# Kernel optimization log

Hardware: AMD Instinct MI355X
Metric: run time of the kernel (lower is better)

The kernel has to match this reference:

```python
import jax, jax.numpy as jnp
import numpy as np

N = 16384
E = 524288
F_IN, F_HID, F_OUT = 128, 256, 128
EPS = 1e-5


def setup_inputs() -> dict:
    key = jax.random.key(0)
    ks = jax.random.split(key, 8)
    x = jax.random.normal(ks[0], (N, F_IN), dtype=jnp.float32)
    edge_index = jax.random.randint(ks[1], (2, E), 0, N, dtype=jnp.int64)
    edge_weight = jax.random.uniform(ks[2], (E,), dtype=jnp.float32)
    # Linear params stored as [in, out] (y = x @ W + b; same math as torch Linear)
    W1_w = jax.random.normal(ks[3], (F_IN, F_HID), dtype=jnp.float32) / np.sqrt(F_IN)
    W1_b = jnp.zeros((F_HID,), dtype=jnp.float32)
    W2_w = jax.random.normal(ks[4], (F_HID, F_OUT), dtype=jnp.float32) / np.sqrt(F_HID)
    W2_b = jnp.zeros((F_OUT,), dtype=jnp.float32)
    ln_g = jnp.ones((F_HID,), dtype=jnp.float32)
    ln_b = jnp.zeros((F_HID,), dtype=jnp.float32)
    return {"x": x, "edge_index": edge_index, "edge_weight": edge_weight,
            "W1_w": W1_w, "W1_b": W1_b, "W2_w": W2_w, "W2_b": W2_b,
            "ln_g": ln_g, "ln_b": ln_b}


def _layernorm(h, g, b):
    mu = jnp.mean(h, axis=-1, keepdims=True)
    var = jnp.var(h, axis=-1, keepdims=True)
    return (h - mu) * jax.lax.rsqrt(var + EPS) * g + b


def reference(x, edge_index, edge_weight, W1_w, W1_b, W2_w, W2_b, ln_g, ln_b):
    n = x.shape[0]
    adj = jnp.zeros((n, n), dtype=x.dtype).at[edge_index[0], edge_index[1]].set(edge_weight)
    adj = adj + jnp.eye(n, dtype=x.dtype)
    degree = jnp.clip(adj.sum(axis=1, keepdims=True), 1.0, None)
    adj = adj / degree
    h = jnp.matmul(adj, x) @ W1_w + W1_b          # [N, F_HID]
    h = jax.nn.relu(_layernorm(h, ln_g, ln_b))
    # dropout is identity in eval mode
    out = jnp.matmul(adj, h) @ W2_w + W2_b        # [N, F_OUT]
    return out
```

## Files before the change

kernel.cpp:

```cpp
#include <hip/hip_runtime.h>

#define N_NODES 16384
#define F_IN    128
#define F_HID   256
#define F_OUT   128
#define LN_EPS  1e-5f
#define CAP     128
#define H0STR   136
#define H1STR   264
#define REPSTR  132

typedef __attribute__((ext_vector_type(8))) short bf16x8;
typedef __attribute__((ext_vector_type(4))) float f32x4;
typedef __attribute__((ext_vector_type(4))) int   i32x4;

__device__ __forceinline__ unsigned short bf16rne(float f) {
    unsigned u = __float_as_uint(f);
    unsigned r = (u + 0x7fffu + ((u >> 16) & 1u)) >> 16;
    return (unsigned short)r;
}
__device__ __forceinline__ float bf_lo(unsigned v) { return __uint_as_float(v << 16); }
__device__ __forceinline__ float bf_hi(unsigned v) { return __uint_as_float(v & 0xffff0000u); }

__global__ void pre_small_kernel(int* __restrict__ cur, const unsigned* __restrict__ ei,
                                 int* __restrict__ mode) {
    int b = blockIdx.x, t = threadIdx.x;
    if (b < 64) {
        cur[b * 256 + t] = 0;
    } else {
        __shared__ int nz;
        if (t == 0) nz = 0;
        __syncthreads();
        for (int it = 0; it < 4; ++it) {
            int idx = 2 * (t + it * 256) + 1;
            if (ei[idx] != 0u) nz = 1;
        }
        __syncthreads();
        if (t == 0) *mode = (nz == 0) ? 1 : 0;
    }
}

__global__ void prep_fill_kernel(const void* __restrict__ ei, const int* __restrict__ mode,
                                 int* __restrict__ cur, int2* __restrict__ ed, int E, int nF,
                                 const float* __restrict__ x, unsigned short* __restrict__ xb,
                                 const float* __restrict__ W1, unsigned short* __restrict__ W1t,
                                 const float* __restrict__ W2, unsigned short* __restrict__ W2t) {
    int b = blockIdx.x, t = threadIdx.x;
    if (b < nF) {
        int base = b * 1024 + t;
        int m = *mode;
#pragma unroll
        for (int u = 0; u < 4; ++u) {
            int e = base + u * 256;
            if (e >= E) continue;
            int r, c;
            if (m) {
                const long long* p = (const long long*)ei;
                r = (int)p[e]; c = (int)p[e + E];
            } else {
                const int* p = (const int*)ei;
                r = p[e]; c = p[e + E];
            }
            if (((unsigned)r | (unsigned)c) >= N_NODES) continue;
            int pos = atomicAdd(&cur[r], 1);
            if (pos < CAP) ed[r * CAP + pos] = make_int2(c, e);
        }
    } else if (b < nF + 2048) {
        int i = ((b - nF) * 256 + t) * 4;
        float4 v = *(const float4*)&x[i];
        ushort4 o;
        o.x = bf16rne(v.x); o.y = bf16rne(v.y); o.z = bf16rne(v.z); o.w = bf16rne(v.w);
        *(ushort4*)&xb[i] = o;
    } else if (b < nF + 2176) {
        int id = (b - nF - 2048) * 256 + t;
        int n = id >> 7, k = id & 127;
        W1t[id] = bf16rne(W1[(size_t)k * F_HID + n]);
    } else {
        int id = (b - nF - 2176) * 256 + t;
        int n = id >> 8, k = id & 255;
        W2t[id] = bf16rne(W2[(size_t)k * F_OUT + n]);
    }
}

__launch_bounds__(1024, 8)
__global__ void agg_mlp_kernel(const float* __restrict__ ew, int* __restrict__ cur,
                               int2* __restrict__ ed, float* __restrict__ invdeg,
                               const unsigned* __restrict__ xb,
                               const unsigned short* __restrict__ W1t,
                               const unsigned short* __restrict__ W2t,
                               const float* __restrict__ b1,
                               const float* __restrict__ ln_g, const float* __restrict__ ln_b,
                               unsigned short* __restrict__ h2b) {
    __shared__ int   scol[16][CAP];
    __shared__ int   seid[16][CAP];
    __shared__ float sw[16][CAP];
    __shared__ unsigned short H0[16 * H0STR];
    __shared__ unsigned short H1[16 * H1STR];
    __shared__ float red[2][16][16];

    int t = threadIdx.x, wave = t >> 6, lane = t & 63;
    int lnid = lane & 15, quad = lane >> 4;
    int half = lane >> 5, hl = lane & 31;
    int Rbase = blockIdx.x * 16;
    int r = Rbase + wave;

    int d = cur[r];
    if (d > CAP) d = CAP;
    int dpad = (d + 15) & ~15;
    int2* row = ed + (size_t)r * CAP;
    for (int i = lane; i < d; i += 64) {
        int2 e = row[i];
        scol[wave][i] = e.x;
        seid[wave][i] = e.y;
    }
    for (int i = d + lane; i < dpad; i += 64) {
        scol[wave][i] = -2;
        seid[wave][i] = 0;
    }
    asm volatile("s_waitcnt lgkmcnt(0)" ::: "memory");

    float wsum = 0.0f;
    for (int i = lane; i < d; i += 64) {
        int myc = scol[wave][i], mye = seid[wave][i];
        bool kill = false;
        for (int jb = 0; jb < dpad; jb += 16) {
            const int* cb = &scol[wave][jb];
            const int* eb = &seid[wave][jb];
            i32x4 c0 = *(const i32x4*)(cb);
            i32x4 c1 = *(const i32x4*)(cb + 4);
            i32x4 c2 = *(const i32x4*)(cb + 8);
            i32x4 c3 = *(const i32x4*)(cb + 12);
            i32x4 e0 = *(const i32x4*)(eb);
            i32x4 e1 = *(const i32x4*)(eb + 4);
            i32x4 e2 = *(const i32x4*)(eb + 8);
            i32x4 e3 = *(const i32x4*)(eb + 12);
            kill |= (c0.x == myc && e0.x > mye);
            kill |= (c0.y == myc && e0.y > mye);
            kill |= (c0.z == myc && e0.z > mye);
            kill |= (c0.w == myc && e0.w > mye);
            kill |= (c1.x == myc && e1.x > mye);
            kill |= (c1.y == myc && e1.y > mye);
            kill |= (c1.z == myc && e1.z > mye);
            kill |= (c1.w == myc && e1.w > mye);
            kill |= (c2.x == myc && e2.x > mye);
            kill |= (c2.y == myc && e2.y > mye);
            kill |= (c2.z == myc && e2.z > mye);
            kill |= (c2.w == myc && e2.w > mye);
            kill |= (c3.x == myc && e3.x > mye);
            kill |= (c3.y == myc && e3.y > mye);
            kill |= (c3.z == myc && e3.z > mye);
            kill |= (c3.w == myc && e3.w > mye);
        }
        float w = kill ? 0.0f : ew[mye];
        sw[wave][i] = w;
        row[i] = make_int2(myc, __float_as_int(w));
        wsum += w;
    }
    asm volatile("s_waitcnt lgkmcnt(0)" ::: "memory");
    for (int off = 32; off; off >>= 1) wsum += __shfl_xor(wsum, off, 64);
    float inv = 1.0f / (1.0f + wsum);
    if (lane == 0) { invdeg[r] = inv; cur[r] = d; }

    const uint2* xb2 = (const uint2*)xb;
    uint2 sv = xb2[(size_t)r * 32 + hl];
    float selfw = half ? 0.0f : 1.0f;
    float a0 = selfw * bf_lo(sv.x), a1 = selfw * bf_hi(sv.x);
    float a2 = selfw * bf_lo(sv.y), a3 = selfw * bf_hi(sv.y);
    int j = 0;
    for (; j + 16 <= d; j += 16) {
        int c[8]; float w[8]; uint2 v[8];
#pragma unroll
        for (int u = 0; u < 8; ++u) {
            c[u] = scol[wave][j + 2 * u + half];
            w[u] = sw[wave][j + 2 * u + half];
        }
#pragma unroll
        for (int u = 0; u < 8; ++u) v[u] = xb2[(size_t)c[u] * 32 + hl];
#pragma unroll
        for (int u = 0; u < 8; ++u) {
            a0 += w[u] * bf_lo(v[u].x); a1 += w[u] * bf_hi(v[u].x);
            a2 += w[u] * bf_lo(v[u].y); a3 += w[u] * bf_hi(v[u].y);
        }
    }
    for (; j + 2 <= d; j += 2) {
        int cc = scol[wave][j + half];
        float w = sw[wave][j + half];
        uint2 v = xb2[(size_t)cc * 32 + hl];
        a0 += w * bf_lo(v.x); a1 += w * bf_hi(v.x);
        a2 += w * bf_lo(v.y); a3 += w * bf_hi(v.y);
    }
    if (j < d) {
        int cc = scol[wave][j];
        float w = half ? 0.0f : sw[wave][j];
        uint2 v = xb2[(size_t)cc * 32 + hl];
        a0 += w * bf_lo(v.x); a1 += w * bf_hi(v.x);
        a2 += w * bf_lo(v.y); a3 += w * bf_hi(v.y);
    }
    a0 += __shfl_xor(a0, 32, 64); a1 += __shfl_xor(a1, 32, 64);
    a2 += __shfl_xor(a2, 32, 64); a3 += __shfl_xor(a3, 32, 64);
    if (half == 0) {
        unsigned w0 = ((unsigned)bf16rne(a1 * inv) << 16) | (unsigned)bf16rne(a0 * inv);
        unsigned w1 = ((unsigned)bf16rne(a3 * inv) << 16) | (unsigned)bf16rne(a2 * inv);
        *(uint2*)&H0[wave * H0STR + hl * 4] = make_uint2(w0, w1);
    }
    __syncthreads();

    bf16x8 a[4];
#pragma unroll
    for (int ch = 0; ch < 4; ++ch)
        a[ch] = *(const bf16x8*)&H0[lnid * H0STR + ch * 32 + quad * 8];
    f32x4 acc = {0.0f, 0.0f, 0.0f, 0.0f};
    {
        const unsigned short* wrow = &W1t[(size_t)(wave * 16 + lnid) * F_IN];
#pragma unroll
        for (int ch = 0; ch < 4; ++ch) {
            bf16x8 b = *(const bf16x8*)&wrow[ch * 32 + quad * 8];
            acc = __builtin_amdgcn_mfma_f32_16x16x32_bf16(a[ch], b, acc, 0, 0, 0);
        }
    }
    float s[4], q[4];
    {
        float bv = b1[wave * 16 + lnid];
#pragma unroll
        for (int rr = 0; rr < 4; ++rr) {
            float v = acc[rr] + bv;
            acc[rr] = v;
            s[rr] = v; q[rr] = v * v;
        }
    }
#pragma unroll
    for (int rr = 0; rr < 4; ++rr)
        for (int off = 1; off < 16; off <<= 1) {
            s[rr] += __shfl_xor(s[rr], off, 64);
            q[rr] += __shfl_xor(q[rr], off, 64);
        }
    if (lnid == 0) {
#pragma unroll
        for (int rr = 0; rr < 4; ++rr) {
            red[0][wave][quad * 4 + rr] = s[rr];
            red[1][wave][quad * 4 + rr] = q[rr];
        }
    }
    __syncthreads();
    float mean[4], rinv[4];
#pragma unroll
    for (int rr = 0; rr < 4; ++rr) {
        int rowi = quad * 4 + rr;
        float S = 0.0f, Q = 0.0f;
#pragma unroll
        for (int w2 = 0; w2 < 16; ++w2) { S += red[0][w2][rowi]; Q += red[1][w2][rowi]; }
        mean[rr] = S * (1.0f / F_HID);
        float var = Q * (1.0f / F_HID) - mean[rr] * mean[rr];
        rinv[rr] = rsqrtf(var + LN_EPS);
    }
    {
        int c = wave * 16 + lnid;
        float g = ln_g[c], bb = ln_b[c];
#pragma unroll
        for (int rr = 0; rr < 4; ++rr) {
            float v = fmaxf((acc[rr] - mean[rr]) * rinv[rr] * g + bb, 0.0f);
            H1[(quad * 4 + rr) * H1STR + c] = bf16rne(v);
        }
    }
    __syncthreads();

    unsigned short* rep = H0;
    if (wave < 8) {
        bf16x8 a2[8];
#pragma unroll
        for (int ch = 0; ch < 8; ++ch)
            a2[ch] = *(const bf16x8*)&H1[lnid * H1STR + ch * 32 + quad * 8];
        f32x4 c2 = {0.0f, 0.0f, 0.0f, 0.0f};
        const unsigned short* wrow = &W2t[(size_t)(wave * 16 + lnid) * F_HID];
#pragma unroll
        for (int ch = 0; ch < 8; ++ch) {
            bf16x8 b = *(const bf16x8*)&wrow[ch * 32 + quad * 8];
            c2 = __builtin_amdgcn_mfma_f32_16x16x32_bf16(a2[ch], b, c2, 0, 0, 0);
        }
#pragma unroll
        for (int rr = 0; rr < 4; ++rr)
            rep[(quad * 4 + rr) * REPSTR + wave * 16 + lnid] = bf16rne(c2[rr]);
    }
    __syncthreads();

    if (t < 512) {
        int m = t >> 5, cg = t & 31;
        *(ushort4*)&h2b[(size_t)(Rbase + m) * F_OUT + cg * 4] =
            *(const ushort4*)&rep[m * REPSTR + cg * 4];
    }
}

__global__ void spmm2_kernel(const unsigned* __restrict__ xb, const int* __restrict__ cur,
                             const int2* __restrict__ ed, const float* __restrict__ invdeg,
                             const float* __restrict__ bias, float* __restrict__ outp) {
    int wave = threadIdx.x >> 6, lane = threadIdx.x & 63;
    int half = lane >> 5, hl = lane & 31;
    int r = blockIdx.x * 4 + wave;
    const int2* row = ed + (size_t)r * CAP;
    const uint2* xb2 = (const uint2*)xb;
    int d = cur[r];
    if (d > CAP) d = CAP;
    uint2 sv = xb2[(size_t)r * 32 + hl];
    float selfw = half ? 0.0f : 1.0f;
    float a0 = selfw * bf_lo(sv.x), a1 = selfw * bf_hi(sv.x);
    float a2 = selfw * bf_lo(sv.y), a3 = selfw * bf_hi(sv.y);
    int j = 0;
    for (; j + 16 <= d; j += 16) {
        int2 q[8]; uint2 v[8];
#pragma unroll
        for (int u = 0; u < 8; ++u) q[u] = row[j + 2 * u + half];
#pragma unroll
        for (int u = 0; u < 8; ++u) v[u] = xb2[(size_t)q[u].x * 32 + hl];
#pragma unroll
        for (int u = 0; u < 8; ++u) {
            float w = __int_as_float(q[u].y);
            a0 += w * bf_lo(v[u].x); a1 += w * bf_hi(v[u].x);
            a2 += w * bf_lo(v[u].y); a3 += w * bf_hi(v[u].y);
        }
    }
    for (; j + 2 <= d; j += 2) {
        int2 q = row[j + half];
        uint2 v = xb2[(size_t)q.x * 32 + hl];
        float w = __int_as_float(q.y);
        a0 += w * bf_lo(v.x); a1 += w * bf_hi(v.x);
        a2 += w * bf_lo(v.y); a3 += w * bf_hi(v.y);
    }
    if (j < d) {
        int2 q = row[j];
        float w = half ? 0.0f : __int_as_float(q.y);
        uint2 v = xb2[(size_t)q.x * 32 + hl];
        a0 += w * bf_lo(v.x); a1 += w * bf_hi(v.x);
        a2 += w * bf_lo(v.y); a3 += w * bf_hi(v.y);
    }
    a0 += __shfl_xor(a0, 32, 64); a1 += __shfl_xor(a1, 32, 64);
    a2 += __shfl_xor(a2, 32, 64); a3 += __shfl_xor(a3, 32, 64);
    if (half == 0) {
        float inv = invdeg[r];
        float4 o;
        o.x = a0 * inv + bias[4 * hl];     o.y = a1 * inv + bias[4 * hl + 1];
        o.z = a2 * inv + bias[4 * hl + 2]; o.w = a3 * inv + bias[4 * hl + 3];
        ((float4*)outp)[(size_t)r * 32 + hl] = o;
    }
}

extern "C" void kernel_launch(void* const* d_in, const int* in_sizes, int n_in,
                              void* d_out, int out_size, void* d_ws, size_t ws_size,
                              hipStream_t stream) {
    const float* x   = (const float*)d_in[0];
    const void*  ei  = d_in[1];
    const float* ew  = (const float*)d_in[2];
    const float* W1  = (const float*)d_in[3];
    const float* b1  = (const float*)d_in[4];
    const float* W2  = (const float*)d_in[5];
    const float* b2  = (const float*)d_in[6];
    const float* lng = (const float*)d_in[7];
    const float* lnb = (const float*)d_in[8];
    float* out = (float*)d_out;
    int E = in_sizes[2];

    char* w = (char*)d_ws;
    size_t off = 0;
    auto take = [&](size_t bytes) -> char* {
        char* p = w + off;
        off += (bytes + 255) & ~(size_t)255;
        return p;
    };
    int*   cur    = (int*)take((size_t)N_NODES * 4);
    float* invdeg = (float*)take((size_t)N_NODES * 4);
    int2*  ed     = (int2*)take((size_t)N_NODES * CAP * 8);
    unsigned short* xb  = (unsigned short*)take((size_t)N_NODES * F_IN * 2);
    unsigned short* h2b = (unsigned short*)take((size_t)N_NODES * F_OUT * 2);
    unsigned short* W1t = (unsigned short*)take((size_t)F_IN * F_HID * 2);
    unsigned short* W2t = (unsigned short*)take((size_t)F_HID * F_OUT * 2);
    int*   mode   = (int*)take(4);

    int nF = (E + 1023) / 1024;
    pre_small_kernel<<<65, 256, 0, stream>>>(cur, (const unsigned*)ei, mode);
    prep_fill_kernel<<<nF + 2304, 256, 0, stream>>>(ei, mode, cur, ed, E, nF,
                                                    x, xb, W1, W1t, W2, W2t);
    agg_mlp_kernel<<<N_NODES / 16, 1024, 0, stream>>>(ew, cur, ed, invdeg,
                                                      (const unsigned*)xb, W1t, W2t,
                                                      b1, lng, lnb, h2b);
    spmm2_kernel<<<N_NODES / 4, 256, 0, stream>>>((const unsigned*)h2b, cur, ed, invdeg,
                                                  b2, out);
}
```

Measured before the change: 188.2 us.

## Split bf16 feature matrices into two column planes for gather locality

Stores the bf16 x and h2 feature matrices as two 64-column planes, so each plane is half the size and more likely to stay cached during random neighbor gathers. Both SpMM passes now loop over the two planes, gathering 4-byte words instead of 8-byte words. The second SpMM is rebuilt with 1024-thread blocks that stage edge columns and weights in shared memory before gathering. The cost is twice the index/weight LDS reads, an extra pass over the edge lists, and narrower per-lane loads.

```diff
diff --git a/kernel.cpp b/kernel.cpp
--- a/kernel.cpp
+++ b/kernel.cpp
@@ -9,6 +9,7 @@
 #define H0STR   136
 #define H1STR   264
 #define REPSTR  132
+#define PLANEU  (N_NODES * 32)
 
 typedef __attribute__((ext_vector_type(8))) short bf16x8;
 typedef __attribute__((ext_vector_type(4))) float f32x4;
@@ -70,7 +71,9 @@
         float4 v = *(const float4*)&x[i];
         ushort4 o;
         o.x = bf16rne(v.x); o.y = bf16rne(v.y); o.z = bf16rne(v.z); o.w = bf16rne(v.w);
-        *(ushort4*)&xb[i] = o;
+        int n = i >> 7, f = i & 127;
+        int p = f >> 6, fo = f & 63;
+        *(ushort4*)&xb[(size_t)p * (N_NODES * 64) + n * 64 + fo] = o;
     } else if (b < nF + 2176) {
         int id = (b - nF - 2048) * 256 + t;
         int n = id >> 7, k = id & 127;
@@ -161,49 +164,47 @@
     float inv = 1.0f / (1.0f + wsum);
     if (lane == 0) { invdeg[r] = inv; cur[r] = d; }
 
-    const uint2* xb2 = (const uint2*)xb;
-    uint2 sv = xb2[(size_t)r * 32 + hl];
     float selfw = half ? 0.0f : 1.0f;
-    float a0 = selfw * bf_lo(sv.x), a1 = selfw * bf_hi(sv.x);
-    float a2 = selfw * bf_lo(sv.y), a3 = selfw * bf_hi(sv.y);
-    int j = 0;
-    for (; j + 16 <= d; j += 16) {
-        int c[8]; float w[8]; uint2 v[8];
-#pragma unroll
-        for (int u = 0; u < 8; ++u) {
-            c[u] = scol[wave][j + 2 * u + half];
-            w[u] = sw[wave][j + 2 * u + half];
-        }
-#pragma unroll
-        for (int u = 0; u < 8; ++u) v[u] = xb2[(size_t)c[u] * 32 + hl];
-#pragma unroll
-        for (int u = 0; u < 8; ++u) {
-            a0 += w[u] * bf_lo(v[u].x); a1 += w[u] * bf_hi(v[u].x);
-            a2 += w[u] * bf_lo(v[u].y); a3 += w[u] * bf_hi(v[u].y);
-        }
-    }
-    for (; j + 2 <= d; j += 2) {
-        int cc = scol[wave][j + half];
-        float w = sw[wave][j + half];
-        uint2 v = xb2[(size_t)cc * 32 + hl];
-        a0 += w * bf_lo(v.x); a1 += w * bf_hi(v.x);
-        a2 += w * bf_lo(v.y); a3 += w * bf_hi(v.y);
-    }
-    if (j < d) {
-        int cc = scol[wave][j];
-        float w = half ? 0.0f : sw[wave][j];
-        uint2 v = xb2[(size_t)cc * 32 + hl];
-        a0 += w * bf_lo(v.x); a1 += w * bf_hi(v.x);
-        a2 += w * bf_lo(v.y); a3 += w * bf_hi(v.y);
-    }
-    a0 += __shfl_xor(a0, 32, 64); a1 += __shfl_xor(a1, 32, 64);
-    a2 += __shfl_xor(a2, 32, 64); a3 += __shfl_xor(a3, 32, 64);
-    if (half == 0) {
-        unsigned w0 = ((unsigned)bf16rne(a1 * inv) << 16) | (unsigned)bf16rne(a0 * inv);
-        unsigned w1 = ((unsigned)bf16rne(a3 * inv) << 16) | (unsigned)bf16rne(a2 * inv);
-        *(uint2*)&H0[wave * H0STR + hl * 4] = make_uint2(w0, w1);
-    }
-    __syncthreads();
+#pragma unroll 1
+    for (int p = 0; p < 2; ++p) {
+        const unsigned* xp = xb + (size_t)p * PLANEU;
+        unsigned sv = xp[r * 32 + hl];
+        float a0 = selfw * bf_lo(sv), a1 = selfw * bf_hi(sv);
+        int j = 0;
+        for (; j + 16 <= d; j += 16) {
+            int c[8]; float w[8]; unsigned v[8];
+#pragma unroll
+            for (int u = 0; u < 8; ++u) {
+                c[u] = scol[wave][j + 2 * u + half];
+                w[u] = sw[wave][j + 2 * u + half];
+            }
+#pragma unroll
+            for (int u = 0; u < 8; ++u) v[u] = xp[c[u] * 32 + hl];
+#pragma unroll
+            for (int u = 0; u < 8; ++u) {
+                a0 += w[u] * bf_lo(v[u]); a1 += w[u] * bf_hi(v[u]);
+            }
+        }
+        for (; j + 2 <= d; j += 2) {
+            int cc = scol[wave][j + half];
+            float w = sw[wave][j + half];
+            unsigned v = xp[cc * 32 + hl];
+            a0 += w * bf_lo(v); a1 += w * bf_hi(v);
+        }
+        if (j < d) {
+            int cc = scol[wave][j];
+            float w = half ? 0.0f : sw[wave][j];
+            unsigned v = xp[cc * 32 + hl];
+            a0 += w * bf_lo(v); a1 += w * bf_hi(v);
+        }
+        a0 += __shfl_xor(a0, 32, 64);
+        a1 += __shfl_xor(a1, 32, 64);
+        if (half == 0) {
+            unsigned w0 = ((unsigned)bf16rne(a1 * inv) << 16) | (unsigned)bf16rne(a0 * inv);
+            *(unsigned*)&H0[wave * H0STR + p * 64 + hl * 2] = w0;
+        }
+        __syncthreads();
+    }
 
     bf16x8 a[4];
 #pragma unroll
@@ -285,61 +286,75 @@
 
     if (t < 512) {
         int m = t >> 5, cg = t & 31;
-        *(ushort4*)&h2b[(size_t)(Rbase + m) * F_OUT + cg * 4] =
+        int p = cg >> 4, fo = (cg & 15) * 4;
+        *(ushort4*)&h2b[(size_t)p * (N_NODES * 64) + (size_t)(Rbase + m) * 64 + fo] =
             *(const ushort4*)&rep[m * REPSTR + cg * 4];
     }
 }
 
+__launch_bounds__(1024, 8)
 __global__ void spmm2_kernel(const unsigned* __restrict__ xb, const int* __restrict__ cur,
                              const int2* __restrict__ ed, const float* __restrict__ invdeg,
                              const float* __restrict__ bias, float* __restrict__ outp) {
-    int wave = threadIdx.x >> 6, lane = threadIdx.x & 63;
+    __shared__ int   scol[16][CAP];
+    __shared__ float sw[16][CAP];
+    int t = threadIdx.x, wave = t >> 6, lane = t & 63;
     int half = lane >> 5, hl = lane & 31;
-    int r = blockIdx.x * 4 + wave;
+    int r = blockIdx.x * 16 + wave;
     const int2* row = ed + (size_t)r * CAP;
-    const uint2* xb2 = (const uint2*)xb;
     int d = cur[r];
     if (d > CAP) d = CAP;
-    uint2 sv = xb2[(size_t)r * 32 + hl];
+    for (int i = lane; i < d; i += 64) {
+        int2 e = row[i];
+        scol[wave][i] = e.x;
+        sw[wave][i] = __int_as_float(e.y);
+    }
+    asm volatile("s_waitcnt lgkmcnt(0)" ::: "memory");
+
+    float inv = invdeg[r];
     float selfw = half ? 0.0f : 1.0f;
-    float a0 = selfw * bf_lo(sv.x), a1 = selfw * bf_hi(sv.x);
-    float a2 = selfw * bf_lo(sv.y), a3 = selfw * bf_hi(sv.y);
-    int j = 0;
-    for (; j + 16 <= d; j += 16) {
-        int2 q[8]; uint2 v[8];
-#pragma unroll
-        for (int u = 0; u < 8; ++u) q[u] = row[j + 2 * u + half];
-#pragma unroll
-        for (int u = 0; u < 8; ++u) v[u] = xb2[(size_t)q[u].x * 32 + hl];
-#pragma unroll
-        for (int u = 0; u < 8; ++u) {
-            float w = __int_as_float(q[u].y);
-            a0 += w * bf_lo(v[u].x); a1 += w * bf_hi(v[u].x);
-            a2 += w * bf_lo(v[u].y); a3 += w * bf_hi(v[u].y);
-        }
-    }
-    for (; j + 2 <= d; j += 2) {
-        int2 q = row[j + half];
-        uint2 v = xb2[(size_t)q.x * 32 + hl];
-        float w = __int_as_float(q.y);
-        a0 += w * bf_lo(v.x); a1 += w * bf_hi(v.x);
-        a2 += w * bf_lo(v.y); a3 += w * bf_hi(v.y);
-    }
-    if (j < d) {
-        int2 q = row[j];
-        float w = half ? 0.0f : __int_as_float(q.y);
-        uint2 v = xb2[(size_t)q.x * 32 + hl];
-        a0 += w * bf_lo(v.x); a1 += w * bf_hi(v.x);
-        a2 += w * bf_lo(v.y); a3 += w * bf_hi(v.y);
-    }
-    a0 += __shfl_xor(a0, 32, 64); a1 += __shfl_xor(a1, 32, 64);
-    a2 += __shfl_xor(a2, 32, 64); a3 += __shfl_xor(a3, 32, 64);
-    if (half == 0) {
-        float inv = invdeg[r];
-        float4 o;
-        o.x = a0 * inv + bias[4 * hl];     o.y = a1 * inv + bias[4 * hl + 1];
-        o.z = a2 * inv + bias[4 * hl + 2]; o.w = a3 * inv + bias[4 * hl + 3];
-        ((float4*)outp)[(size_t)r * 32 + hl] = o;
+#pragma unroll 1
+    for (int p = 0; p < 2; ++p) {
+        const unsigned* xp = xb + (size_t)p * PLANEU;
+        unsigned sv = xp[r * 32 + hl];
+        float a0 = selfw * bf_lo(sv), a1 = selfw * bf_hi(sv);
+        int j = 0;
+        for (; j + 16 <= d; j += 16) {
+            int c[8]; float w[8]; unsigned v[8];
+#pragma unroll
+            for (int u = 0; u < 8; ++u) {
+                c[u] = scol[wave][j + 2 * u + half];
+                w[u] = sw[wave][j + 2 * u + half];
+            }
+#pragma unroll
+            for (int u = 0; u < 8; ++u) v[u] = xp[c[u] * 32 + hl];
+#pragma unroll
+            for (int u = 0; u < 8; ++u) {
+                a0 += w[u] * bf_lo(v[u]); a1 += w[u] * bf_hi(v[u]);
+            }
+        }
+        for (; j + 2 <= d; j += 2) {
+            int cc = scol[wave][j + half];
+            float w = sw[wave][j + half];
+            unsigned v = xp[cc * 32 + hl];
+            a0 += w * bf_lo(v); a1 += w * bf_hi(v);
+        }
+        if (j < d) {
+            int cc = scol[wave][j];
+            float w = half ? 0.0f : sw[wave][j];
+            unsigned v = xp[cc * 32 + hl];
+            a0 += w * bf_lo(v); a1 += w * bf_hi(v);
+        }
+        a0 += __shfl_xor(a0, 32, 64);
+        a1 += __shfl_xor(a1, 32, 64);
+        if (half == 0) {
+            int f = p * 64 + 2 * hl;
+            float2 o;
+            o.x = a0 * inv + bias[f];
+            o.y = a1 * inv + bias[f + 1];
+            *(float2*)&outp[(size_t)r * F_OUT + f] = o;
+        }
+        __syncthreads();
     }
 }
 
@@ -381,6 +396,6 @@
     agg_mlp_kernel<<<N_NODES / 16, 1024, 0, stream>>>(ew, cur, ed, invdeg,
                                                       (const unsigned*)xb, W1t, W2t,
                                                       b1, lng, lnb, h2b);
-    spmm2_kernel<<<N_NODES / 4, 256, 0, stream>>>((const unsigned*)h2b, cur, ed, invdeg,
-                                                  b2, out);
-}
+    spmm2_kernel<<<N_NODES / 16, 1024, 0, stream>>>((const unsigned*)h2b, cur, ed, invdeg,
+                                                    b2, out);
+}
```

After: 195.0 us. 3.6% more time.
